# Optimization experiments

Measured on AMD Instinct MI355X. Metric: run time of the kernel, lower is better.

Reference implementation:

```python
import jax, jax.numpy as jnp
import numpy as np

N, E, IN, H, OUT, K = 50000, 800000, 128, 64, 64, 1024


def setup_inputs() -> dict:
    key = jax.random.key(0)
    ks = jax.random.split(key, 8)
    x = jax.random.normal(ks[0], (N, IN), dtype=jnp.float32)
    edge_index = jax.random.randint(ks[1], (2, E), 0, N, dtype=jnp.int32)
    cluster_id = jax.random.randint(ks[2], (N,), 0, K, dtype=jnp.int32)
    W1 = jax.random.normal(ks[3], (IN, H), dtype=jnp.float32) / np.float32(np.sqrt(IN))
    b1 = jnp.zeros((H,), jnp.float32)
    W2 = jax.random.normal(ks[4], (H, OUT), dtype=jnp.float32) / np.float32(np.sqrt(H))
    b2 = jnp.zeros((OUT,), jnp.float32)
    W_skip = jax.random.normal(ks[5], (H, OUT), dtype=jnp.float32) / np.float32(np.sqrt(H))
    b_skip = jnp.zeros((OUT,), jnp.float32)
    alpha = jnp.full((1,), 1.5, jnp.float32)
    return dict(x=x, edge_index=edge_index, cluster_id=cluster_id, W1=W1, b1=b1,
                W2=W2, b2=b2, W_skip=W_skip, b_skip=b_skip, alpha=alpha)


def gcn_conv_sparse(x, src, dst, n, W, b):
    # PyG GCNConv: transform, then D^{-1/2}(A+I)D^{-1/2} aggregation, then bias.
    h = x @ W  # [n, F_out]
    deg = jax.ops.segment_sum(jnp.ones_like(src, dtype=h.dtype), dst, num_segments=n) + 1.0
    dinv = jax.lax.rsqrt(deg)
    norm = dinv[src] * dinv[dst]  # [E]
    agg = jax.ops.segment_sum(h[src] * norm[:, None], dst, num_segments=n)
    agg = agg + (dinv * dinv)[:, None] * h  # self-loop term
    return agg + b


def reference(x, edge_index, cluster_id, W1, b1, W2, b2, W_skip, b_skip, alpha):
    src, dst = edge_index[0], edge_index[1]
    # conv1 + ReLU (dropout is identity in eval mode)
    x1 = jax.nn.relu(gcn_conv_sparse(x, src, dst, N, W1, b1))  # [N, H]

    # pool_by_partition: scatter-mean node features into K clusters
    sums = jax.ops.segment_sum(x1, cluster_id, num_segments=K)  # [K, H]
    counts = jnp.maximum(jax.ops.segment_sum(jnp.ones((N,), x1.dtype), cluster_id, num_segments=K), 1.0)
    x_p = sums / counts[:, None]

    # deduped pooled edges, self-loops removed == dense 0/1 adjacency with zero diag (K small)
    cu, cv = cluster_id[src], cluster_id[dst]
    A = jnp.zeros((K, K), x1.dtype).at[cu, cv].set(1.0)
    A = A * (1.0 - jnp.eye(K, dtype=x1.dtype))
    A_hat = A + jnp.eye(K, dtype=x1.dtype)
    deg_p = jnp.sum(A_hat, axis=0)  # in-degree at target (PyG computes deg on col)
    dinv_p = jax.lax.rsqrt(deg_p)
    A_norm = dinv_p[:, None] * A_hat * dinv_p[None, :]  # [src, dst]
    h_p = x_p @ W2
    x_p2 = jnp.einsum('st,sf->tf', A_norm, h_p) + b2  # [K, OUT]

    # gather-broadcast + strengthened skip head
    up = x_p2[cluster_id]  # [N, OUT]
    skip = x1 @ W_skip + b_skip
    logits = up + jax.nn.relu(alpha)[0] * skip
    return logits
```

## Files before the change

### kernel.cpp

```cpp
#include <hip/hip_runtime.h>

#define NN 50000
#define NE 800000
#define FIN 128
#define FH 64
#define FOUT 64
#define KC 1024
#define CAP 64
#define EPB 4096
#define NCH ((NE + EPB - 1) / EPB)
#define NBK ((NN + 255) / 256)

typedef unsigned char  u8;
typedef unsigned short u16;
typedef unsigned int   u32;


__global__ __launch_bounds__(256) void k_count(const int* __restrict__ dst,
                                               int* __restrict__ bktcnt) {
    __shared__ int hist[256];
    int t = threadIdx.x;
    hist[t] = 0;
    __syncthreads();
    int e0 = blockIdx.x * EPB, e1 = min(NE, e0 + EPB);
    for (int e = e0 + t; e < e1; e += 256)
        atomicAdd(&hist[dst[e] >> 8], 1);
    __syncthreads();
    if (t < NBK && hist[t]) atomicAdd(&bktcnt[t], hist[t]);
}

__global__ __launch_bounds__(256) void k_bscan(const int* __restrict__ bktcnt,
                                               int* __restrict__ bases,
                                               int* __restrict__ gcur) {
    __shared__ int sm[256];
    int t = threadIdx.x;
    int v = (t < NBK) ? bktcnt[t] : 0;
    sm[t] = v;
    __syncthreads();
    for (int o = 1; o < 256; o <<= 1) {
        int u = (t >= o) ? sm[t - o] : 0;
        __syncthreads();
        sm[t] += u;
        __syncthreads();
    }
    if (t < NBK) { int ex = sm[t] - v; bases[t] = ex; gcur[t] = ex; }
    if (t == NBK) bases[NBK] = sm[255];
}

__global__ __launch_bounds__(256) void k_part(const int* __restrict__ src,
                                              const int* __restrict__ dst,
                                              const int* __restrict__ cid,
                                              int* __restrict__ gcur,
                                              u32* __restrict__ bin,
                                              u8* __restrict__ AT) {
    __shared__ int hist[256], off[256], cur[256], gbase[256];
    __shared__ u32 sorted[EPB];
    int t = threadIdx.x;
    hist[t] = 0; cur[t] = 0;
    __syncthreads();
    int e0 = blockIdx.x * EPB, e1 = min(NE, e0 + EPB);
    for (int e = e0 + t; e < e1; e += 256)
        atomicAdd(&hist[dst[e] >> 8], 1);
    __syncthreads();
    int v = hist[t];
    off[t] = v;
    __syncthreads();
    for (int o = 1; o < 256; o <<= 1) {
        int u = (t >= o) ? off[t - o] : 0;
        __syncthreads();
        off[t] += u;
        __syncthreads();
    }
    int ex = off[t] - v;
    __syncthreads();
    off[t] = ex;
    __syncthreads();
    for (int e = e0 + t; e < e1; e += 256) {
        int d = dst[e], s = src[e];
        int b = d >> 8, local = d & 255;
        int cu = cid[s], cv = cid[d];
        if (cu != cv) AT[(size_t)cv * KC + cu] = 1;
        int p = off[b] + atomicAdd(&cur[b], 1);
        sorted[p] = ((u32)b << 24) | ((u32)local << 16) | (u32)s;
    }
    __syncthreads();
    if (t < NBK && hist[t]) gbase[t] = atomicAdd(&gcur[t], hist[t]);
    __syncthreads();
    int cnt = e1 - e0;
    for (int i = t; i < cnt; i += 256) {
        u32 e = sorted[i];
        int b = e >> 24;
        bin[gbase[b] + (i - off[b])] = e;
    }
}

__global__ __launch_bounds__(256) void k_slots(const int* __restrict__ bases,
                                               const u32* __restrict__ bin,
                                               const int* __restrict__ cid,
                                               int* __restrict__ deg,
                                               float* __restrict__ dinv,
                                               int* __restrict__ counts,
                                               u16* __restrict__ slots) {
    __shared__ u16 sbuf[256 * CAP];
    __shared__ int c_lds[256];
    int t = threadIdx.x, b = blockIdx.x;
    c_lds[t] = 0;
    __syncthreads();
    int s0 = bases[b], s1 = bases[b + 1];
    for (int i = s0 + t; i < s1; i += 256) {
        u32 e = bin[i];
        int local = (e >> 16) & 255;
        int pos = atomicAdd(&c_lds[local], 1);
        if (pos < CAP) sbuf[local * CAP + pos] = (u16)(e & 0xffffu);
    }
    __syncthreads();
    int node = b * 256 + t;
    if (node < NN) {
        int d = c_lds[t];
        deg[node] = d;
        dinv[node] = rsqrtf((float)d + 1.0f);
        atomicAdd(&counts[cid[node]], 1);
    }
    int rows = min(256, NN - b * 256);
    int n4 = rows * (CAP * 2 / 16);
    const uint4* sb4 = (const uint4*)sbuf;
    uint4* gs4 = (uint4*)(slots + (size_t)b * 256 * CAP);
    for (int j = t; j < n4; j += 256) gs4[j] = sb4[j];
}

__global__ __launch_bounds__(256) void k_degp(const u8* __restrict__ AT,
                                              float* __restrict__ dinvp) {
    __shared__ int sm[4];
    int t = blockIdx.x;
    int lane = threadIdx.x & 63, w = threadIdx.x >> 6;
    const u32* row = (const u32*)(AT + (size_t)t * KC);
    int s = __popc(row[threadIdx.x]);
    for (int o = 32; o; o >>= 1) s += __shfl_down(s, o);
    if (lane == 0) sm[w] = s;
    __syncthreads();
    if (threadIdx.x == 0)
        dinvp[t] = rsqrtf(1.0f + (float)(sm[0] + sm[1] + sm[2] + sm[3]));
}

__global__ __launch_bounds__(256) void k_gemm1(const float* __restrict__ x,
                                               const float* __restrict__ W1,
                                               const float* __restrict__ dinv,
                                               float* __restrict__ h) {
    __shared__ float Ws[FIN * FH];
    __shared__ float Xs[32 * FIN];
    int t = threadIdx.x;
    int row_base = blockIdx.x * 32;
    for (int i = t; i < FIN * FH; i += 256) Ws[i] = W1[i];
    {
        const float4* x4 = (const float4*)x;
        float4* xs4 = (float4*)Xs;
        for (int i = t; i < 32 * 32; i += 256) {
            int r = i >> 5, k4 = i & 31;
            int row = row_base + r;
            float4 v = make_float4(0.f, 0.f, 0.f, 0.f);
            if (row < NN) v = x4[(size_t)row * 32 + k4];
            xs4[i] = v;
        }
    }
    __syncthreads();
    int col = t & 31, grp = t >> 5;
    int r0 = grp * 4;
    const float4* p0 = (const float4*)&Xs[(r0 + 0) * FIN];
    const float4* p1 = (const float4*)&Xs[(r0 + 1) * FIN];
    const float4* p2 = (const float4*)&Xs[(r0 + 2) * FIN];
    const float4* p3 = (const float4*)&Xs[(r0 + 3) * FIN];
    float acc00 = 0.f, acc01 = 0.f, acc10 = 0.f, acc11 = 0.f;
    float acc20 = 0.f, acc21 = 0.f, acc30 = 0.f, acc31 = 0.f;
#pragma unroll 2
    for (int k4 = 0; k4 < FIN / 4; ++k4) {
        float4 a0 = p0[k4], a1 = p1[k4], a2 = p2[k4], a3 = p3[k4];
        const float* wp = &Ws[(k4 * 4) * FH + col];
        float w00 = wp[0],          w01 = wp[32];
        float w10 = wp[FH],         w11 = wp[FH + 32];
        float w20 = wp[2 * FH],     w21 = wp[2 * FH + 32];
        float w30 = wp[3 * FH],     w31 = wp[3 * FH + 32];
        acc00 = fmaf(a0.x, w00, fmaf(a0.y, w10, fmaf(a0.z, w20, fmaf(a0.w, w30, acc00))));
        acc01 = fmaf(a0.x, w01, fmaf(a0.y, w11, fmaf(a0.z, w21, fmaf(a0.w, w31, acc01))));
        acc10 = fmaf(a1.x, w00, fmaf(a1.y, w10, fmaf(a1.z, w20, fmaf(a1.w, w30, acc10))));
        acc11 = fmaf(a1.x, w01, fmaf(a1.y, w11, fmaf(a1.z, w21, fmaf(a1.w, w31, acc11))));
        acc20 = fmaf(a2.x, w00, fmaf(a2.y, w10, fmaf(a2.z, w20, fmaf(a2.w, w30, acc20))));
        acc21 = fmaf(a2.x, w01, fmaf(a2.y, w11, fmaf(a2.z, w21, fmaf(a2.w, w31, acc21))));
        acc30 = fmaf(a3.x, w00, fmaf(a3.y, w10, fmaf(a3.z, w20, fmaf(a3.w, w30, acc30))));
        acc31 = fmaf(a3.x, w01, fmaf(a3.y, w11, fmaf(a3.z, w21, fmaf(a3.w, w31, acc31))));
    }
    int row0 = row_base + r0;
    if (row0 + 0 < NN) { float di = dinv[row0 + 0]; h[(size_t)(row0 + 0) * FH + col] = di * acc00; h[(size_t)(row0 + 0) * FH + col + 32] = di * acc01; }
    if (row0 + 1 < NN) { float di = dinv[row0 + 1]; h[(size_t)(row0 + 1) * FH + col] = di * acc10; h[(size_t)(row0 + 1) * FH + col + 32] = di * acc11; }
    if (row0 + 2 < NN) { float di = dinv[row0 + 2]; h[(size_t)(row0 + 2) * FH + col] = di * acc20; h[(size_t)(row0 + 2) * FH + col + 32] = di * acc21; }
    if (row0 + 3 < NN) { float di = dinv[row0 + 3]; h[(size_t)(row0 + 3) * FH + col] = di * acc30; h[(size_t)(row0 + 3) * FH + col + 32] = di * acc31; }
}

__global__ __launch_bounds__(256) void k_gather(const int* __restrict__ deg,
                                                const u16* __restrict__ slots,
                                                const float* __restrict__ dinv,
                                                const float* __restrict__ h,
                                                const float* __restrict__ b1,
                                                const int* __restrict__ cid,
                                                float* __restrict__ x1,
                                                float* __restrict__ sums) {
    int lane = threadIdx.x & 63;
    int node = blockIdx.x * 4 + (threadIdx.x >> 6);
    if (node >= NN) return;
    int q = lane >> 4, fl = lane & 15;
    const float4* h4 = (const float4*)h;
    int cnt = min(deg[node], CAP);
    const u16* cp = slots + (size_t)node * CAP;
    float4 acc = make_float4(0.f, 0.f, 0.f, 0.f);
    {
        int s = (lane < cnt) ? (int)cp[lane] : 0;
        int nFull = cnt >> 2;
        for (int j = 0; j < nFull; ++j) {
            int ss = __shfl(s, j * 4 + q);
            float4 hv = h4[(size_t)ss * 16 + fl];
            acc.x += hv.x; acc.y += hv.y; acc.z += hv.z; acc.w += hv.w;
        }
        int tail = cnt & 3;
        if (tail) {
            int ss = __shfl(s, nFull * 4 + q);
            float m = (q < tail) ? 1.f : 0.f;
            float4 hv = h4[(size_t)ss * 16 + fl];
            acc.x = fmaf(m, hv.x, acc.x);
            acc.y = fmaf(m, hv.y, acc.y);
            acc.z = fmaf(m, hv.z, acc.z);
            acc.w = fmaf(m, hv.w, acc.w);
        }
    }
    acc.x += __shfl_xor(acc.x, 16); acc.y += __shfl_xor(acc.y, 16);
    acc.z += __shfl_xor(acc.z, 16); acc.w += __shfl_xor(acc.w, 16);
    acc.x += __shfl_xor(acc.x, 32); acc.y += __shfl_xor(acc.y, 32);
    acc.z += __shfl_xor(acc.z, 32); acc.w += __shfl_xor(acc.w, 32);
    float di = dinv[node];
    float4 hs = h4[(size_t)node * 16 + fl];
    const float4* b14 = (const float4*)b1;
    float4 bb = b14[fl];
    float4 v;
    v.x = fmaxf(fmaf(di, acc.x + hs.x, bb.x), 0.f);
    v.y = fmaxf(fmaf(di, acc.y + hs.y, bb.y), 0.f);
    v.z = fmaxf(fmaf(di, acc.z + hs.z, bb.z), 0.f);
    v.w = fmaxf(fmaf(di, acc.w + hs.w, bb.w), 0.f);
    if (q == 0) ((float4*)x1)[(size_t)node * 16 + fl] = v;
    int c = cid[node];
    float comp = (q == 0) ? v.x : (q == 1) ? v.y : (q == 2) ? v.z : v.w;
    unsafeAtomicAdd(&sums[(size_t)c * FH + fl * 4 + q], comp);
}

__global__ __launch_bounds__(64) void k_pool(const float* __restrict__ sums,
                                             const int* __restrict__ counts,
                                             const float* __restrict__ W2,
                                             const float* __restrict__ dinvp,
                                             float* __restrict__ g) {
    __shared__ float xp[FH];
    int s = blockIdx.x, f = threadIdx.x;
    float cnt = fmaxf((float)counts[s], 1.0f);
    xp[f] = sums[(size_t)s * FH + f] / cnt;
    __syncthreads();
    float acc = 0.f;
    for (int j = 0; j < FH; ++j) acc = fmaf(xp[j], W2[j * FH + f], acc);
    g[(size_t)s * FH + f] = dinvp[s] * acc;
}

__global__ __launch_bounds__(256) void k_xp2(const u8* __restrict__ AT,
                                             const float* __restrict__ g,
                                             const float* __restrict__ dinvp,
                                             const float* __restrict__ b2,
                                             float* __restrict__ xp2) {
    __shared__ float4 sm4[4][16];
    int t = blockIdx.x;
    int lane = threadIdx.x & 63, w = threadIdx.x >> 6;
    int q = lane >> 4, fl = lane & 15;
    const u32* roww = (const u32*)(AT + (size_t)t * KC);
    const float4* g4 = (const float4*)g;
    float4 acc = make_float4(0.f, 0.f, 0.f, 0.f);
    int wb = w * 64;
    u32 wv = roww[wb + lane];
    for (int j = 0; j < 16; ++j) {
        u32 word = __shfl((int)wv, j * 4 + q);
        int sidx = (wb + j * 4 + q) * 4;
#pragma unroll
        for (int b = 0; b < 4; ++b) {
            float a = (float)((word >> (8 * b)) & 255u);
            float4 gv = g4[(size_t)(sidx + b) * 16 + fl];
            acc.x = fmaf(a, gv.x, acc.x);
            acc.y = fmaf(a, gv.y, acc.y);
            acc.z = fmaf(a, gv.z, acc.z);
            acc.w = fmaf(a, gv.w, acc.w);
        }
    }
    acc.x += __shfl_xor(acc.x, 16); acc.y += __shfl_xor(acc.y, 16);
    acc.z += __shfl_xor(acc.z, 16); acc.w += __shfl_xor(acc.w, 16);
    acc.x += __shfl_xor(acc.x, 32); acc.y += __shfl_xor(acc.y, 32);
    acc.z += __shfl_xor(acc.z, 32); acc.w += __shfl_xor(acc.w, 32);
    if (q == 0) sm4[w][fl] = acc;
    __syncthreads();
    if (threadIdx.x < 16) {
        int f = threadIdx.x;
        float4 a0 = sm4[0][f], a1 = sm4[1][f], a2 = sm4[2][f], a3 = sm4[3][f];
        float4 gs = g4[(size_t)t * 16 + f];
        float dp = dinvp[t];
        const float4* b24 = (const float4*)b2;
        float4 bb = b24[f];
        float4 o;
        o.x = fmaf(dp, a0.x + a1.x + a2.x + a3.x + gs.x, bb.x);
        o.y = fmaf(dp, a0.y + a1.y + a2.y + a3.y + gs.y, bb.y);
        o.z = fmaf(dp, a0.z + a1.z + a2.z + a3.z + gs.z, bb.z);
        o.w = fmaf(dp, a0.w + a1.w + a2.w + a3.w + gs.w, bb.w);
        ((float4*)xp2)[(size_t)t * 16 + f] = o;
    }
}

__global__ __launch_bounds__(256) void k_final(const float* __restrict__ x1,
                                               const float* __restrict__ Wsk,
                                               const float* __restrict__ bsk,
                                               const float* __restrict__ xp2,
                                               const int* __restrict__ cid,
                                               const float* __restrict__ alpha,
                                               float* __restrict__ out) {
    __shared__ float Ws[FH * FOUT];
    __shared__ float Xs[32 * FH];
    int t = threadIdx.x;
    int row_base = blockIdx.x * 32;
    for (int i = t; i < FH * FOUT; i += 256) Ws[i] = Wsk[i];
    {
        const float4* x4 = (const float4*)x1;
        float4* xs4 = (float4*)Xs;
        for (int i = t; i < 32 * 16; i += 256) {
            int r = i >> 4, k4 = i & 15;
            int row = row_base + r;
            float4 v = make_float4(0.f, 0.f, 0.f, 0.f);
            if (row < NN) v = x4[(size_t)row * 16 + k4];
            xs4[i] = v;
        }
    }
    __syncthreads();
    float al = fmaxf(alpha[0], 0.f);
    int col = t & 31, grp = t >> 5;
    int r0 = grp * 4;
    const float4* p0 = (const float4*)&Xs[(r0 + 0) * FH];
    const float4* p1 = (const float4*)&Xs[(r0 + 1) * FH];
    const float4* p2 = (const float4*)&Xs[(r0 + 2) * FH];
    const float4* p3 = (const float4*)&Xs[(r0 + 3) * FH];
    float acc00 = 0.f, acc01 = 0.f, acc10 = 0.f, acc11 = 0.f;
    float acc20 = 0.f, acc21 = 0.f, acc30 = 0.f, acc31 = 0.f;
#pragma unroll 2
    for (int k4 = 0; k4 < FH / 4; ++k4) {
        float4 a0 = p0[k4], a1 = p1[k4], a2 = p2[k4], a3 = p3[k4];
        const float* wp = &Ws[(k4 * 4) * FOUT + col];
        float w00 = wp[0],           w01 = wp[32];
        float w10 = wp[FOUT],        w11 = wp[FOUT + 32];
        float w20 = wp[2 * FOUT],    w21 = wp[2 * FOUT + 32];
        float w30 = wp[3 * FOUT],    w31 = wp[3 * FOUT + 32];
        acc00 = fmaf(a0.x, w00, fmaf(a0.y, w10, fmaf(a0.z, w20, fmaf(a0.w, w30, acc00))));
        acc01 = fmaf(a0.x, w01, fmaf(a0.y, w11, fmaf(a0.z, w21, fmaf(a0.w, w31, acc01))));
        acc10 = fmaf(a1.x, w00, fmaf(a1.y, w10, fmaf(a1.z, w20, fmaf(a1.w, w30, acc10))));
        acc11 = fmaf(a1.x, w01, fmaf(a1.y, w11, fmaf(a1.z, w21, fmaf(a1.w, w31, acc11))));
        acc20 = fmaf(a2.x, w00, fmaf(a2.y, w10, fmaf(a2.z, w20, fmaf(a2.w, w30, acc20))));
        acc21 = fmaf(a2.x, w01, fmaf(a2.y, w11, fmaf(a2.z, w21, fmaf(a2.w, w31, acc21))));
        acc30 = fmaf(a3.x, w00, fmaf(a3.y, w10, fmaf(a3.z, w20, fmaf(a3.w, w30, acc30))));
        acc31 = fmaf(a3.x, w01, fmaf(a3.y, w11, fmaf(a3.z, w21, fmaf(a3.w, w31, acc31))));
    }
    float bb0 = bsk[col], bb1 = bsk[col + 32];
    int row0 = row_base + r0;
#pragma unroll
    for (int i = 0; i < 4; ++i) {
        float a0 = (i == 0) ? acc00 : (i == 1) ? acc10 : (i == 2) ? acc20 : acc30;
        float a1 = (i == 0) ? acc01 : (i == 1) ? acc11 : (i == 2) ? acc21 : acc31;
        int row = row0 + i;
        if (row < NN) {
            int c = cid[row];
            out[(size_t)row * FOUT + col]      = xp2[(size_t)c * FOUT + col]      + al * (a0 + bb0);
            out[(size_t)row * FOUT + col + 32] = xp2[(size_t)c * FOUT + col + 32] + al * (a1 + bb1);
        }
    }
}

extern "C" void kernel_launch(void* const* d_in, const int* in_sizes, int n_in,
                              void* d_out, int out_size, void* d_ws, size_t ws_size,
                              hipStream_t stream) {
    const float* x    = (const float*)d_in[0];
    const int*   ei   = (const int*)d_in[1];
    const int*   cid  = (const int*)d_in[2];
    const float* W1   = (const float*)d_in[3];
    const float* b1   = (const float*)d_in[4];
    const float* W2   = (const float*)d_in[5];
    const float* b2   = (const float*)d_in[6];
    const float* Wsk  = (const float*)d_in[7];
    const float* bsk  = (const float*)d_in[8];
    const float* alpha= (const float*)d_in[9];
    float* out = (float*)d_out;
    const int* src = ei;
    const int* dst = ei + NE;

    char* ws = (char*)d_ws;
    size_t cur = 0;
    auto alloc = [&](size_t nb) { cur = (cur + 255) & ~(size_t)255; size_t o = cur; cur += nb; return o; };
    size_t o_sums = alloc((size_t)KC * FH * 4);
    size_t o_AT   = alloc((size_t)KC * KC);
    size_t o_cnt  = alloc((size_t)KC * 4);
    size_t o_bkt  = alloc((size_t)NBK * 4);
    size_t zero_bytes = cur;
    size_t o_base = alloc((size_t)(NBK + 1) * 4);
    size_t o_gcur = alloc((size_t)NBK * 4);
    size_t o_bin  = alloc((size_t)NE * 4);
    size_t o_slot = alloc((size_t)NN * CAP * 2);
    size_t o_deg  = alloc((size_t)NN * 4);
    size_t o_x1   = alloc((size_t)NN * FH * 4);
    size_t o_h    = alloc((size_t)NN * FH * 4);
    size_t o_dinv = alloc((size_t)NN * 4);
    size_t o_g    = alloc((size_t)KC * FH * 4);
    size_t o_xp2  = alloc((size_t)KC * FH * 4);
    size_t o_dinvp= alloc((size_t)KC * 4);
    (void)ws_size; (void)in_sizes; (void)n_in; (void)out_size;

    float* sums = (float*)(ws + o_sums);
    u8*    AT   = (u8*)(ws + o_AT);
    int*   cnt  = (int*)(ws + o_cnt);
    int*   bkt  = (int*)(ws + o_bkt);
    int*   base = (int*)(ws + o_base);
    int*   gcur = (int*)(ws + o_gcur);
    u32*   bin  = (u32*)(ws + o_bin);
    u16*   slot = (u16*)(ws + o_slot);
    int*   deg  = (int*)(ws + o_deg);
    float* x1   = (float*)(ws + o_x1);
    float* h    = (float*)(ws + o_h);
    float* dinv = (float*)(ws + o_dinv);
    float* g    = (float*)(ws + o_g);
    float* xp2  = (float*)(ws + o_xp2);
    float* dinvp= (float*)(ws + o_dinvp);

    hipMemsetAsync(d_ws, 0, zero_bytes, stream);

    const int NRB = (NN + 31) / 32;
    k_count <<<NCH, 256, 0, stream>>>(dst, bkt);
    k_bscan <<<1, 256, 0, stream>>>(bkt, base, gcur);
    k_part  <<<NCH, 256, 0, stream>>>(src, dst, cid, gcur, bin, AT);
    k_slots <<<NBK, 256, 0, stream>>>(base, bin, cid, deg, dinv, cnt, slot);
    k_degp  <<<KC, 256, 0, stream>>>(AT, dinvp);
    k_gemm1 <<<NRB, 256, 0, stream>>>(x, W1, dinv, h);
    k_gather<<<(NN + 3) / 4, 256, 0, stream>>>(deg, slot, dinv, h, b1, cid, x1, sums);
    k_pool  <<<KC, 64, 0, stream>>>(sums, cnt, W2, dinvp, g);
    k_xp2   <<<KC, 256, 0, stream>>>(AT, g, dinvp, b2, xp2);
    k_final <<<NRB, 256, 0, stream>>>(x1, Wsk, bsk, xp2, cid, alpha, out);
}
```

Measured before the change: 221.2 us.

## Fuse skip-head GEMM into gather kernel and replace final kernel with elementwise add

The skip projection x1 @ W_skip is now computed inside the gather kernel, right after each node's x1 row is produced, using a shared-memory copy of W_skip. The result, already scaled by alpha and with the skip bias added, is written to a buffer. This removes the x1 round trip through global memory. The final kernel becomes a simple vectorised add of that buffer and the gathered pooled features. The cost is a 16KB W_skip load into shared memory for every 4-node block (12.5k blocks), which adds LDS traffic, lowers occupancy and adds a barrier in the gather. The edge-chunk size for the count/partition kernels is also halved.

New measurement: 234.1 us. 5.8% more time.

```diff
diff --git a/kernel.cpp b/kernel.cpp
--- a/kernel.cpp
+++ b/kernel.cpp
@@ -7,7 +7,7 @@
 #define FOUT 64
 #define KC 1024
 #define CAP 64
-#define EPB 4096
+#define EPB 2048
 #define NCH ((NE + EPB - 1) / EPB)
 #define NBK ((NN + 255) / 256)
 
@@ -201,17 +201,26 @@
                                                 const float* __restrict__ h,
                                                 const float* __restrict__ b1,
                                                 const int* __restrict__ cid,
-                                                float* __restrict__ x1,
+                                                const float* __restrict__ Wsk,
+                                                const float* __restrict__ bsk,
+                                                const float* __restrict__ alpha,
+                                                float* __restrict__ skp,
                                                 float* __restrict__ sums) {
-    int lane = threadIdx.x & 63;
-    int node = blockIdx.x * 4 + (threadIdx.x >> 6);
-    if (node >= NN) return;
+    __shared__ float Ws[FH * FOUT];
+    __shared__ float vbuf[4][FH];
+    int t = threadIdx.x;
+    for (int i = t; i < FH * FOUT; i += 256) Ws[i] = Wsk[i];
+    __syncthreads();
+    int lane = t & 63, w = t >> 6;
+    int node = blockIdx.x * 4 + w;
+    bool ok = (node < NN);
     int q = lane >> 4, fl = lane & 15;
     const float4* h4 = (const float4*)h;
-    int cnt = min(deg[node], CAP);
-    const u16* cp = slots + (size_t)node * CAP;
-    float4 acc = make_float4(0.f, 0.f, 0.f, 0.f);
-    {
+    float4 v = make_float4(0.f, 0.f, 0.f, 0.f);
+    if (ok) {
+        int cnt = min(deg[node], CAP);
+        const u16* cp = slots + (size_t)node * CAP;
+        float4 acc = make_float4(0.f, 0.f, 0.f, 0.f);
         int s = (lane < cnt) ? (int)cp[lane] : 0;
         int nFull = cnt >> 2;
         for (int j = 0; j < nFull; ++j) {
@@ -229,24 +238,37 @@
             acc.z = fmaf(m, hv.z, acc.z);
             acc.w = fmaf(m, hv.w, acc.w);
         }
-    }
-    acc.x += __shfl_xor(acc.x, 16); acc.y += __shfl_xor(acc.y, 16);
-    acc.z += __shfl_xor(acc.z, 16); acc.w += __shfl_xor(acc.w, 16);
-    acc.x += __shfl_xor(acc.x, 32); acc.y += __shfl_xor(acc.y, 32);
-    acc.z += __shfl_xor(acc.z, 32); acc.w += __shfl_xor(acc.w, 32);
-    float di = dinv[node];
-    float4 hs = h4[(size_t)node * 16 + fl];
-    const float4* b14 = (const float4*)b1;
-    float4 bb = b14[fl];
-    float4 v;
-    v.x = fmaxf(fmaf(di, acc.x + hs.x, bb.x), 0.f);
-    v.y = fmaxf(fmaf(di, acc.y + hs.y, bb.y), 0.f);
-    v.z = fmaxf(fmaf(di, acc.z + hs.z, bb.z), 0.f);
-    v.w = fmaxf(fmaf(di, acc.w + hs.w, bb.w), 0.f);
-    if (q == 0) ((float4*)x1)[(size_t)node * 16 + fl] = v;
-    int c = cid[node];
-    float comp = (q == 0) ? v.x : (q == 1) ? v.y : (q == 2) ? v.z : v.w;
-    unsafeAtomicAdd(&sums[(size_t)c * FH + fl * 4 + q], comp);
+        acc.x += __shfl_xor(acc.x, 16); acc.y += __shfl_xor(acc.y, 16);
+        acc.z += __shfl_xor(acc.z, 16); acc.w += __shfl_xor(acc.w, 16);
+        acc.x += __shfl_xor(acc.x, 32); acc.y += __shfl_xor(acc.y, 32);
+        acc.z += __shfl_xor(acc.z, 32); acc.w += __shfl_xor(acc.w, 32);
+        float di = dinv[node];
+        float4 hs = h4[(size_t)node * 16 + fl];
+        const float4* b14 = (const float4*)b1;
+        float4 bb = b14[fl];
+        v.x = fmaxf(fmaf(di, acc.x + hs.x, bb.x), 0.f);
+        v.y = fmaxf(fmaf(di, acc.y + hs.y, bb.y), 0.f);
+        v.z = fmaxf(fmaf(di, acc.z + hs.z, bb.z), 0.f);
+        v.w = fmaxf(fmaf(di, acc.w + hs.w, bb.w), 0.f);
+        if (q == 0) {
+            vbuf[w][fl * 4 + 0] = v.x; vbuf[w][fl * 4 + 1] = v.y;
+            vbuf[w][fl * 4 + 2] = v.z; vbuf[w][fl * 4 + 3] = v.w;
+        }
+        int c = cid[node];
+        float comp = (q == 0) ? v.x : (q == 1) ? v.y : (q == 2) ? v.z : v.w;
+        unsafeAtomicAdd(&sums[(size_t)c * FH + fl * 4 + q], comp);
+    }
+    __syncthreads();
+    if (ok) {
+        float acco = 0.f;
+        const float* vp = vbuf[w];
+        const float* wp = &Ws[lane];
+#pragma unroll 8
+        for (int j = 0; j < FH; ++j)
+            acco = fmaf(vp[j], wp[j * FOUT], acco);
+        float al = fmaxf(alpha[0], 0.f);
+        skp[(size_t)node * FOUT + lane] = al * (acco + bsk[lane]);
+    }
 }
 
 __global__ __launch_bounds__(64) void k_pool(const float* __restrict__ sums,
@@ -313,69 +335,17 @@
     }
 }
 
-__global__ __launch_bounds__(256) void k_final(const float* __restrict__ x1,
-                                               const float* __restrict__ Wsk,
-                                               const float* __restrict__ bsk,
-                                               const float* __restrict__ xp2,
-                                               const int* __restrict__ cid,
-                                               const float* __restrict__ alpha,
-                                               float* __restrict__ out) {
-    __shared__ float Ws[FH * FOUT];
-    __shared__ float Xs[32 * FH];
-    int t = threadIdx.x;
-    int row_base = blockIdx.x * 32;
-    for (int i = t; i < FH * FOUT; i += 256) Ws[i] = Wsk[i];
-    {
-        const float4* x4 = (const float4*)x1;
-        float4* xs4 = (float4*)Xs;
-        for (int i = t; i < 32 * 16; i += 256) {
-            int r = i >> 4, k4 = i & 15;
-            int row = row_base + r;
-            float4 v = make_float4(0.f, 0.f, 0.f, 0.f);
-            if (row < NN) v = x4[(size_t)row * 16 + k4];
-            xs4[i] = v;
-        }
-    }
-    __syncthreads();
-    float al = fmaxf(alpha[0], 0.f);
-    int col = t & 31, grp = t >> 5;
-    int r0 = grp * 4;
-    const float4* p0 = (const float4*)&Xs[(r0 + 0) * FH];
-    const float4* p1 = (const float4*)&Xs[(r0 + 1) * FH];
-    const float4* p2 = (const float4*)&Xs[(r0 + 2) * FH];
-    const float4* p3 = (const float4*)&Xs[(r0 + 3) * FH];
-    float acc00 = 0.f, acc01 = 0.f, acc10 = 0.f, acc11 = 0.f;
-    float acc20 = 0.f, acc21 = 0.f, acc30 = 0.f, acc31 = 0.f;
-#pragma unroll 2
-    for (int k4 = 0; k4 < FH / 4; ++k4) {
-        float4 a0 = p0[k4], a1 = p1[k4], a2 = p2[k4], a3 = p3[k4];
-        const float* wp = &Ws[(k4 * 4) * FOUT + col];
-        float w00 = wp[0],           w01 = wp[32];
-        float w10 = wp[FOUT],        w11 = wp[FOUT + 32];
-        float w20 = wp[2 * FOUT],    w21 = wp[2 * FOUT + 32];
-        float w30 = wp[3 * FOUT],    w31 = wp[3 * FOUT + 32];
-        acc00 = fmaf(a0.x, w00, fmaf(a0.y, w10, fmaf(a0.z, w20, fmaf(a0.w, w30, acc00))));
-        acc01 = fmaf(a0.x, w01, fmaf(a0.y, w11, fmaf(a0.z, w21, fmaf(a0.w, w31, acc01))));
-        acc10 = fmaf(a1.x, w00, fmaf(a1.y, w10, fmaf(a1.z, w20, fmaf(a1.w, w30, acc10))));
-        acc11 = fmaf(a1.x, w01, fmaf(a1.y, w11, fmaf(a1.z, w21, fmaf(a1.w, w31, acc11))));
-        acc20 = fmaf(a2.x, w00, fmaf(a2.y, w10, fmaf(a2.z, w20, fmaf(a2.w, w30, acc20))));
-        acc21 = fmaf(a2.x, w01, fmaf(a2.y, w11, fmaf(a2.z, w21, fmaf(a2.w, w31, acc21))));
-        acc30 = fmaf(a3.x, w00, fmaf(a3.y, w10, fmaf(a3.z, w20, fmaf(a3.w, w30, acc30))));
-        acc31 = fmaf(a3.x, w01, fmaf(a3.y, w11, fmaf(a3.z, w21, fmaf(a3.w, w31, acc31))));
-    }
-    float bb0 = bsk[col], bb1 = bsk[col + 32];
-    int row0 = row_base + r0;
-#pragma unroll
-    for (int i = 0; i < 4; ++i) {
-        float a0 = (i == 0) ? acc00 : (i == 1) ? acc10 : (i == 2) ? acc20 : acc30;
-        float a1 = (i == 0) ? acc01 : (i == 1) ? acc11 : (i == 2) ? acc21 : acc31;
-        int row = row0 + i;
-        if (row < NN) {
-            int c = cid[row];
-            out[(size_t)row * FOUT + col]      = xp2[(size_t)c * FOUT + col]      + al * (a0 + bb0);
-            out[(size_t)row * FOUT + col + 32] = xp2[(size_t)c * FOUT + col + 32] + al * (a1 + bb1);
-        }
-    }
+__global__ __launch_bounds__(256) void k_add(const float* __restrict__ skp,
+                                             const float* __restrict__ xp2,
+                                             const int* __restrict__ cid,
+                                             float* __restrict__ out) {
+    int i = blockIdx.x * 256 + threadIdx.x;
+    if (i >= NN * FH / 4) return;
+    int row = i >> 4;
+    int c = cid[row];
+    float4 a = ((const float4*)skp)[i];
+    float4 b = ((const float4*)xp2)[(size_t)c * 16 + (i & 15)];
+    ((float4*)out)[i] = make_float4(a.x + b.x, a.y + b.y, a.z + b.z, a.w + b.w);
 }
 
 extern "C" void kernel_launch(void* const* d_in, const int* in_sizes, int n_in,
@@ -408,7 +378,7 @@
     size_t o_bin  = alloc((size_t)NE * 4);
     size_t o_slot = alloc((size_t)NN * CAP * 2);
     size_t o_deg  = alloc((size_t)NN * 4);
-    size_t o_x1   = alloc((size_t)NN * FH * 4);
+    size_t o_skp  = alloc((size_t)NN * FH * 4);
     size_t o_h    = alloc((size_t)NN * FH * 4);
     size_t o_dinv = alloc((size_t)NN * 4);
     size_t o_g    = alloc((size_t)KC * FH * 4);
@@ -425,7 +395,7 @@
     u32*   bin  = (u32*)(ws + o_bin);
     u16*   slot = (u16*)(ws + o_slot);
     int*   deg  = (int*)(ws + o_deg);
-    float* x1   = (float*)(ws + o_x1);
+    float* skp  = (float*)(ws + o_skp);
     float* h    = (float*)(ws + o_h);
     float* dinv = (float*)(ws + o_dinv);
     float* g    = (float*)(ws + o_g);
@@ -434,15 +404,16 @@
 
     hipMemsetAsync(d_ws, 0, zero_bytes, stream);
 
-    const int NRB = (NN + 31) / 32;
     k_count <<<NCH, 256, 0, stream>>>(dst, bkt);
     k_bscan <<<1, 256, 0, stream>>>(bkt, base, gcur);
     k_part  <<<NCH, 256, 0, stream>>>(src, dst, cid, gcur, bin, AT);
     k_slots <<<NBK, 256, 0, stream>>>(base, bin, cid, deg, dinv, cnt, slot);
     k_degp  <<<KC, 256, 0, stream>>>(AT, dinvp);
+    const int NRB = (NN + 31) / 32;
     k_gemm1 <<<NRB, 256, 0, stream>>>(x, W1, dinv, h);
-    k_gather<<<(NN + 3) / 4, 256, 0, stream>>>(deg, slot, dinv, h, b1, cid, x1, sums);
+    k_gather<<<(NN + 3) / 4, 256, 0, stream>>>(deg, slot, dinv, h, b1, cid,
+                                               Wsk, bsk, alpha, skp, sums);
     k_pool  <<<KC, 64, 0, stream>>>(sums, cnt, W2, dinvp, g);
     k_xp2   <<<KC, 256, 0, stream>>>(AT, g, dinvp, b2, xp2);
-    k_final <<<NRB, 256, 0, stream>>>(x1, Wsk, bsk, xp2, cid, alpha, out);
-}
+    k_add   <<<(NN * FH / 4 + 255) / 256, 256, 0, stream>>>(skp, xp2, cid, out);
+}
```
